# Performance work log

Hardware: AMD Instinct MI355X
Metric: run time of the kernel (lower is better)

The kernel has to match this reference:

```python
import jax, jax.numpy as jnp
import numpy as np
from jax import lax

ANGRES = 5


def _conv(x, w, stride=(1, 1), pad=((1, 1), (1, 1)), dil=(1, 1)):
    return lax.conv_general_dilated(x, w, stride, pad, rhs_dilation=dil,
                                    dimension_numbers=('NCHW', 'OIHW', 'NCHW'))


def _lrelu(x):
    return jnp.where(x >= 0, x, 0.1 * x)


def _block_s(x, w):
    # SAI input: split into 5x5 grid of (sh,sw) views, conv each view, emit MacPI-interleaved layout
    B, C, H, W = x.shape
    sh, sw = H // 5, W // 5
    p = x.reshape(B, C, 5, sh, 5, sw).transpose(0, 2, 4, 1, 3, 5).reshape(B * 25, C, sh, sw)
    y = _conv(p, w).reshape(B, 5, 5, C, sh, sw)
    # (B,bi,bj,C,sh,sw) -> (B,C,sh,bi,sw,bj) -> (B,C,H,W)   [torch permute(0,3,4,1,5,2)]
    return y.transpose(0, 3, 4, 1, 5, 2).reshape(B, C, H, W)


def _block_a(x, w):
    # MacPI input: conv each 5x5 macropixel independently (zero pad at block edges)
    B, C, H, W = x.shape
    nh, nw = H // 5, W // 5
    p = x.reshape(B, C, nh, 5, nw, 5).transpose(0, 2, 4, 1, 3, 5).reshape(B * nh * nw, C, 5, 5)
    y = _conv(p, w)
    return y.reshape(B, nh, nw, C, 5, 5).transpose(0, 3, 1, 4, 2, 5).reshape(B, C, H, W)


def _epi(x, w1, w2, a):
    # EPI conv: [1,3a] kernel, stride [1,a], pad [0,a]; then 1x1 to a*C; then 1D pixel shuffle on W
    y = _lrelu(_conv(x, w1, stride=(1, a), pad=((0, 0), (a, a))))
    y = _lrelu(_conv(y, w2, pad=((0, 0), (0, 0))))
    B, aC, H, Wa = y.shape
    C = aC // a
    return y.reshape(B, a, C, H, Wa).transpose(0, 2, 3, 4, 1).reshape(B, C, H, Wa * a)


def _att_fuse(buf, alpha, gamma, beta, eps=1e-5):
    # covariance-based GLU attention over the N=4 branches
    B, NC, H, W = buf.shape
    N = 4
    C = NC // N
    x5 = buf.reshape(B, N, C, H, W)
    xr = x5.reshape(B, N, C * H * W)
    M = xr.shape[-1]
    xc = xr - jnp.mean(xr, axis=-1, keepdims=True)
    cov = jnp.einsum('bnm,bkm->bnk', xc, xc) * (alpha / (M - 1))  # [B,N,N]
    norm = cov / jnp.sqrt(jnp.mean(cov * cov, axis=(1, 2), keepdims=True) + eps)
    g = gamma * norm + beta
    att = g * jax.nn.sigmoid(g)  # GLU of duplicated halves
    out = jnp.einsum('bnk,bkm->bnm', att, xr).reshape(B, N, C, H, W) + x5
    return out.reshape(B, NC, H, W)


def _mac2sai(x, a):
    B, C, HU, WV = x.shape
    h, w = HU // a, WV // a
    return x.reshape(B, C, a, h, a, w).transpose(0, 1, 3, 5, 2, 4).reshape(B, C, h * a, w * a)


def _tsfefb(x, x1, ws, wa, we1, we2, al, ga, be, wf1, wf2, a):
    feaSpa = _lrelu(_block_s(x1, ws))
    feaAng = _lrelu(_block_a(x, wa))
    feaH = _epi(x, we1, we2, a)
    feaV = jnp.transpose(_epi(jnp.transpose(x, (0, 1, 3, 2)), we1, we2, a), (0, 1, 3, 2))
    buf = jnp.concatenate([feaSpa, feaAng, feaH, feaV], axis=1)
    out = _att_fuse(buf, al, ga, be)
    y = _lrelu(_conv(out, wf1, pad=((0, 0), (0, 0))))
    y = _conv(y, wf2, pad=((a, a), (a, a)), dil=(a, a))
    return y + x


def setup_inputs() -> dict:
    key = jax.random.key(0)
    ks = jax.random.split(key, 12)
    B, C, a, n = 4, 64, ANGRES, 4
    H = W = a * 32  # 160

    def w(k, shape):
        fan_in = float(np.prod(shape[2:]))
        return jax.random.normal(k, shape, jnp.float32) / np.float32(np.sqrt(fan_in))

    return {
        'x': jax.random.normal(ks[0], (B, C, H, W), jnp.float32),
        'x1': jax.random.normal(ks[1], (B, C, H, W), jnp.float32),
        'w_spa': w(ks[2], (n, C, C, 3, 3)),
        'w_ang': w(ks[3], (n, C, C, 3, 3)),
        'w_epi1': w(ks[4], (n, C, C, 1, 3 * a)),
        'w_epi2': w(ks[5], (n, a * C, C, 1, 1)),
        'alpha': jnp.ones((n,), jnp.float32),
        'gamma': 0.1 * jax.random.normal(ks[6], (n,), jnp.float32),
        'beta': 0.1 * jax.random.normal(ks[7], (n,), jnp.float32),
        'w_fuse1': w(ks[8], (n, C, 4 * C, 1, 1)),
        'w_fuse2': w(ks[9], (n, C, C, 3, 3)),
    }


def reference(x, x1, w_spa, w_ang, w_epi1, w_epi2, alpha, gamma, beta, w_fuse1, w_fuse2):
    a = ANGRES
    buf, buf1 = x, x1
    for i in range(w_spa.shape[0]):
        buf = _tsfefb(buf, buf1, w_spa[i], w_ang[i], w_epi1[i], w_epi2[i],
                      alpha[i], gamma[i], beta[i], w_fuse1[i], w_fuse2[i], a)
        buf1 = _mac2sai(buf, a)
    return buf
```

## Files before the change

### kernel.cpp

```cpp
#include <hip/hip_runtime.h>

__device__ __forceinline__ float lrelu(float v){ return v >= 0.f ? v : 0.1f*v; }


__global__ __launch_bounds__(256) void k_spa(const float* __restrict__ buf1, const float* __restrict__ w,
                                             float* __restrict__ out){
  const int P = blockIdx.x;
  const int within = P >> 3, cog = within & 7, tsel = within >> 3;
  const int tg = (P & 7)*25 + tsel;
  const int b = tg / 50, r2 = tg % 50;
  const int view = r2 >> 1, half = r2 & 1;
  const int bi = view / 5, bj = view % 5;
  const int th0 = half*16;
  const int tid = threadIdx.x;
  __shared__ float plane[2][18*38];
  for (int idx=tid; idx<2*18*38; idx+=256) ((float*)plane)[idx]=0.f;
  float acc[2][8];
  #pragma unroll
  for (int k=0;k<2;k++)
    #pragma unroll
    for (int c=0;c<8;c++) acc[k][c]=0.f;
  const float* src = buf1 + (size_t)b*1638400 + bi*32*160 + bj*32;
  const float* wb = w + (size_t)(cog*8)*576;
  const int sr = tid >> 3, sq = (tid & 7)*4;
  const int vr = th0 - 1 + sr;
  const bool rowok = (tid < 144) && ((unsigned)vr < 32u);
  __syncthreads();
  if (rowok)
    *(float4*)&plane[0][sr*38 + 4 + sq] = *(const float4*)(src + vr*160 + sq);
  __syncthreads();
  const int lr = tid >> 5, c = tid & 31;
  for (int ci=0; ci<64; ci++){
    float4 nx;
    const bool ld = rowok && (ci < 63);
    if (ld) nx = *(const float4*)(src + (size_t)(ci+1)*25600 + vr*160 + sq);
    const float* P2 = plane[ci & 1];
    float t0[9], t1[9];
    {
      const float* pp = &P2[lr*38 + c + 3];
      t0[0]=pp[0];  t0[1]=pp[1];  t0[2]=pp[2];
      t0[3]=pp[38]; t0[4]=pp[39]; t0[5]=pp[40];
      t0[6]=pp[76]; t0[7]=pp[77]; t0[8]=pp[78];
      const float* qq = pp + 8*38;
      t1[0]=qq[0];  t1[1]=qq[1];  t1[2]=qq[2];
      t1[3]=qq[38]; t1[4]=qq[39]; t1[5]=qq[40];
      t1[6]=qq[76]; t1[7]=qq[77]; t1[8]=qq[78];
    }
    #pragma unroll
    for (int co=0;co<8;co++){
      const float* wp = wb + (size_t)co*576 + ci*9;
      float w0=wp[0],w1=wp[1],w2=wp[2],w3=wp[3],w4=wp[4],w5=wp[5],w6=wp[6],w7=wp[7],w8=wp[8];
      acc[0][co] += t0[0]*w0+t0[1]*w1+t0[2]*w2+t0[3]*w3+t0[4]*w4
                  + t0[5]*w5+t0[6]*w6+t0[7]*w7+t0[8]*w8;
      acc[1][co] += t1[0]*w0+t1[1]*w1+t1[2]*w2+t1[3]*w3+t1[4]*w4
                  + t1[5]*w5+t1[6]*w6+t1[7]*w7+t1[8]*w8;
    }
    if (ld) *(float4*)&plane[(ci+1)&1][sr*38 + 4 + sq] = nx;
    __syncthreads();
  }
  #pragma unroll
  for (int k=0;k<2;k++){
    int si = th0 + lr + k*8;
    int h = si*5 + bi, wq = c*5 + bj;
    #pragma unroll
    for (int co=0;co<8;co++){
      int ch = b*64 + cog*8 + co;
      out[(size_t)ch*25600 + h*160 + wq] = lrelu(acc[k][co]);
    }
  }
}

__global__ __launch_bounds__(320) void k_ang(const float* __restrict__ bufA, const float* __restrict__ w,
                                             float* __restrict__ out){
  const int P = blockIdx.x;
  const int within = P >> 3, cog = within & 15, tsel = within >> 4;
  const int tg = (P & 7)*8 + tsel;
  const int b = tg >> 4, mip = tg & 15;
  const int tid = threadIdx.x;
  __shared__ float lds[2][2240];
  for (int i=tid; i<2*2240; i+=320) ((float*)lds)[i] = 0.f;

  const int u = tid >> 6, mi_l = (tid >> 5) & 1, mp = tid & 31;
  int offm[3], offa[3];
  #pragma unroll
  for (int du=0; du<3; du++){
    offm[du] = mi_l*896 + (u+du)*128 + mp*4;
    offa[du] = 1792 + mi_l*224 + (u+du)*32 + mp;
  }
  const bool st1 = tid < 80;
  int sdst0[4], sdst1[4];
  const int rr0 = tid/40,       q0 = tid%40;
  const int rr1 = (tid+320)/40, q1 = (tid+320)%40;
  #pragma unroll
  for (int j=0;j<4;j++){
    int g = q0*4+j, mpw = g/5, vw = g - mpw*5;
    int miw = rr0/5, uw = rr0 - miw*5;
    sdst0[j] = (vw<4) ? (miw*896 + (1+uw)*128 + mpw*4 + vw)
                      : (1792 + miw*224 + (1+uw)*32 + mpw);
    g = q1*4+j; mpw = g/5; vw = g - mpw*5;
    miw = rr1/5; uw = rr1 - miw*5;
    sdst1[j] = (vw<4) ? (miw*896 + (1+uw)*128 + mpw*4 + vw)
                      : (1792 + miw*224 + (1+uw)*32 + mpw);
  }
  const float* src = bufA + (size_t)b*1638400 + (size_t)(mip*10)*160;
  const float* wb = w + (size_t)(cog*4)*576;

  float acc[4][5];
  #pragma unroll
  for (int co=0;co<4;co++)
    #pragma unroll
    for (int v=0;v<5;v++) acc[co][v]=0.f;

  __syncthreads();
  {
    float4 x0 = *(const float4*)(src + rr0*160 + q0*4);
    lds[0][sdst0[0]]=x0.x; lds[0][sdst0[1]]=x0.y; lds[0][sdst0[2]]=x0.z; lds[0][sdst0[3]]=x0.w;
    if (st1){
      float4 x1 = *(const float4*)(src + rr1*160 + q1*4);
      lds[0][sdst1[0]]=x1.x; lds[0][sdst1[1]]=x1.y; lds[0][sdst1[2]]=x1.z; lds[0][sdst1[3]]=x1.w;
    }
  }
  __syncthreads();
  for (int ci=0; ci<64; ci++){
    float4 n0, n1;
    if (ci < 63){
      n0 = *(const float4*)(src + (size_t)(ci+1)*25600 + rr0*160 + q0*4);
      if (st1) n1 = *(const float4*)(src + (size_t)(ci+1)*25600 + rr1*160 + q1*4);
    }
    const float* Pb = lds[ci & 1];
    float c[3][5];
    #pragma unroll
    for (int du=0;du<3;du++){
      float4 m = *(const float4*)&Pb[offm[du]];
      c[du][0]=m.x; c[du][1]=m.y; c[du][2]=m.z; c[du][3]=m.w;
      c[du][4]=Pb[offa[du]];
    }
    #pragma unroll
    for (int co=0;co<4;co++){
      const float* wp = wb + (size_t)co*576 + ci*9;
      float w0=wp[0],w1=wp[1],w2=wp[2],w3=wp[3],w4=wp[4],w5=wp[5],w6=wp[6],w7=wp[7],w8=wp[8];
      acc[co][0] += c[0][0]*w1 + c[0][1]*w2
                  + c[1][0]*w4 + c[1][1]*w5
                  + c[2][0]*w7 + c[2][1]*w8;
      acc[co][1] += c[0][0]*w0 + c[0][1]*w1 + c[0][2]*w2
                  + c[1][0]*w3 + c[1][1]*w4 + c[1][2]*w5
                  + c[2][0]*w6 + c[2][1]*w7 + c[2][2]*w8;
      acc[co][2] += c[0][1]*w0 + c[0][2]*w1 + c[0][3]*w2
                  + c[1][1]*w3 + c[1][2]*w4 + c[1][3]*w5
                  + c[2][1]*w6 + c[2][2]*w7 + c[2][3]*w8;
      acc[co][3] += c[0][2]*w0 + c[0][3]*w1 + c[0][4]*w2
                  + c[1][2]*w3 + c[1][3]*w4 + c[1][4]*w5
                  + c[2][2]*w6 + c[2][3]*w7 + c[2][4]*w8;
      acc[co][4] += c[0][3]*w0 + c[0][4]*w1
                  + c[1][3]*w3 + c[1][4]*w4
                  + c[2][3]*w6 + c[2][4]*w7;
    }
    if (ci < 63){
      float* Q = lds[(ci+1)&1];
      Q[sdst0[0]]=n0.x; Q[sdst0[1]]=n0.y; Q[sdst0[2]]=n0.z; Q[sdst0[3]]=n0.w;
      if (st1){ Q[sdst1[0]]=n1.x; Q[sdst1[1]]=n1.y; Q[sdst1[2]]=n1.z; Q[sdst1[3]]=n1.w; }
    }
    __syncthreads();
  }
  const int h = (mip*2 + mi_l)*5 + u;
  const int wc0 = mp*5;
  #pragma unroll
  for (int co=0;co<4;co++){
    int ch = b*64 + cog*4 + co;
    float* op = out + (size_t)ch*25600 + (size_t)h*160 + wc0;
    op[0]=lrelu(acc[co][0]); op[1]=lrelu(acc[co][1]); op[2]=lrelu(acc[co][2]);
    op[3]=lrelu(acc[co][3]); op[4]=lrelu(acc[co][4]);
  }
}

__global__ __launch_bounds__(320) void k_epi(const float* __restrict__ bufA, const float* __restrict__ we1,
                                             const float* __restrict__ we2, float* __restrict__ out){
  const int b = blockIdx.x / 160, hw = blockIdx.x % 160;
  const int tid = threadIdx.x;
  __shared__ float rowp[64*176];
  __shared__ float y1s[64*32];
  for (int ft=tid; ft<2560; ft+=320){
    int ci = ft/40, xq = (ft - ci*40)*4;
    *(float4*)&rowp[ci*176 + 8 + xq] =
      *(const float4*)(bufA + (size_t)b*1638400 + (size_t)ci*25600 + (size_t)hw*160 + xq);
  }
  for (int idx=tid; idx<64*16; idx+=320){
    int ci = idx>>4, j = idx&15;
    rowp[ci*176 + (j<8 ? j : 160+j)] = 0.f;
  }
  __syncthreads();
  if (tid < 256){
    const int co = tid >> 2, wv0 = (tid & 3)*8;
    const int a0 = 2 + wv0*5;
    float acc[8];
    #pragma unroll
    for (int j=0;j<8;j++) acc[j]=0.f;
    const float* wp0 = we1 + (size_t)co*960;
    for (int ci=0; ci<64; ci++){
      float fl[52];
      const float* rp = &rowp[ci*176 + a0];
      #pragma unroll
      for (int m=0;m<26;m++) *(float2*)&fl[2*m] = *(const float2*)&rp[2*m];
      const float* wp = wp0 + ci*15;
      #pragma unroll
      for (int t=0;t<15;t++){
        float wt = wp[t];
        #pragma unroll
        for (int j=0;j<8;j++) acc[j] += fl[1 + j*5 + t]*wt;
      }
    }
    #pragma unroll
    for (int j=0;j<8;j++) y1s[co*32 + wv0 + j] = lrelu(acc[j]);
  }
  __syncthreads();
  {
    const int oc = tid, kk = oc >> 6, c = oc & 63;
    float a2[32];
    #pragma unroll
    for (int wv=0;wv<32;wv++) a2[wv]=0.f;
    const float* wp = we2 + (size_t)oc*64;
    for (int ci=0; ci<64; ci++){
      float wt = wp[ci];
      const float* yp = &y1s[ci*32];
      #pragma unroll
      for (int wv=0; wv<32; wv++) a2[wv] += yp[wv]*wt;
    }
    float* y2s = rowp;
    #pragma unroll
    for (int wv=0; wv<32; wv++) y2s[c*164 + wv*5 + kk] = lrelu(a2[wv]);
  }
  __syncthreads();
  {
    const float* y2s = rowp;
    for (int k=0;k<8;k++){
      int f = (tid + k*320)*4;
      int c = f/160, rr = f - c*160;
      *(float4*)(out + (size_t)(b*64+c)*25600 + (size_t)hw*160 + rr) = *(const float4*)&y2s[c*164+rr];
    }
  }
}

__global__ __launch_bounds__(256) void k_permV(const float* __restrict__ tmp, float* __restrict__ dst){
  const int bc = blockIdx.x;
  const int ti = blockIdx.y / 5, tj = blockIdx.y % 5;
  const int hw0 = ti*32, r0 = tj*32;
  const int lx = threadIdx.x & 31, ly = threadIdx.x >> 5;
  __shared__ float tile[32][33];
  const float* in = tmp + (size_t)bc*25600;
  float* outp = dst + (size_t)bc*25600;
  for (int yy=ly; yy<32; yy+=8)
    tile[yy][lx] = in[(size_t)(hw0+yy)*160 + r0 + lx];
  __syncthreads();
  for (int yy=ly; yy<32; yy+=8)
    outp[(size_t)(r0+yy)*160 + hw0 + lx] = tile[lx][yy];
}

__global__ __launch_bounds__(256) void k_permM(const float* __restrict__ A, float* __restrict__ dst){
  const int bc = blockIdx.x >> 5, hh = blockIdx.x & 31;
  const int tid = threadIdx.x;
  __shared__ float rows[5*160];
  const float* in = A + (size_t)bc*25600;
  if (tid < 200){
    int ai = tid/40, q = (tid - ai*40)*4;
    *(float4*)&rows[ai*160 + q] = *(const float4*)(in + (size_t)(ai*32+hh)*160 + q);
  }
  __syncthreads();
  float* outp = dst + (size_t)bc*25600 + (size_t)hh*800;
  for (int t=tid; t<800; t+=256){
    int ww = t/25, r2 = t - ww*25, ai = r2/5, aj = r2 - ai*5;
    outp[t] = rows[ai*160 + aj*32 + ww];
  }
}

__global__ __launch_bounds__(256) void k_red(const float* __restrict__ b0, const float* __restrict__ b1,
                                             const float* __restrict__ b2, const float* __restrict__ b3,
                                             float* __restrict__ part){
  const int b = blockIdx.y, blk = blockIdx.x;
  const int tid = threadIdx.x;
  const size_t off = (size_t)b*1638400 + (size_t)blk*25600;
  float s0=0,s1=0,s2=0,s3=0;
  float p00=0,p01=0,p02=0,p03=0,p11=0,p12=0,p13=0,p22=0,p23=0,p33=0;
  for (int it=0; it<25; it++){
    size_t m = off + it*1024 + tid*4;
    float4 x0 = *(const float4*)(b0+m);
    float4 x1 = *(const float4*)(b1+m);
    float4 x2 = *(const float4*)(b2+m);
    float4 x3 = *(const float4*)(b3+m);
    s0 += (x0.x+x0.y)+(x0.z+x0.w);
    s1 += (x1.x+x1.y)+(x1.z+x1.w);
    s2 += (x2.x+x2.y)+(x2.z+x2.w);
    s3 += (x3.x+x3.y)+(x3.z+x3.w);
    p00 += x0.x*x0.x+x0.y*x0.y+x0.z*x0.z+x0.w*x0.w;
    p01 += x0.x*x1.x+x0.y*x1.y+x0.z*x1.z+x0.w*x1.w;
    p02 += x0.x*x2.x+x0.y*x2.y+x0.z*x2.z+x0.w*x2.w;
    p03 += x0.x*x3.x+x0.y*x3.y+x0.z*x3.z+x0.w*x3.w;
    p11 += x1.x*x1.x+x1.y*x1.y+x1.z*x1.z+x1.w*x1.w;
    p12 += x1.x*x2.x+x1.y*x2.y+x1.z*x2.z+x1.w*x2.w;
    p13 += x1.x*x3.x+x1.y*x3.y+x1.z*x3.z+x1.w*x3.w;
    p22 += x2.x*x2.x+x2.y*x2.y+x2.z*x2.z+x2.w*x2.w;
    p23 += x2.x*x3.x+x2.y*x3.y+x2.z*x3.z+x2.w*x3.w;
    p33 += x3.x*x3.x+x3.y*x3.y+x3.z*x3.z+x3.w*x3.w;
  }
  float vals[14] = {s0,s1,s2,s3,p00,p01,p02,p03,p11,p12,p13,p22,p23,p33};
  __shared__ float red[4][14];
  int lane = tid & 63, wv = tid >> 6;
  #pragma unroll
  for (int j=0;j<14;j++){
    float v = vals[j];
    #pragma unroll
    for (int o=32;o>0;o>>=1) v += __shfl_down(v,o,64);
    if (lane==0) red[wv][j]=v;
  }
  __syncthreads();
  if (tid<14) part[((size_t)b*64+blk)*16 + tid] = red[0][tid]+red[1][tid]+red[2][tid]+red[3][tid];
}

__global__ __launch_bounds__(256) void k_attW(const float* __restrict__ part,
        const float* __restrict__ alpha, const float* __restrict__ gamma, const float* __restrict__ beta,
        int iblk, const float* __restrict__ wf1, float* __restrict__ Weff){
  const int b = blockIdx.x, tid = threadIdx.x;
  __shared__ float st[14];
  __shared__ float att[16];
  if (tid<14){
    float t=0;
    for (int blk=0;blk<64;blk++) t += part[((size_t)b*64+blk)*16 + tid];
    st[tid]=t;
  }
  __syncthreads();
  if (tid==0){
    const float M = 1638400.f;
    float s[4] = {st[0],st[1],st[2],st[3]};
    float S[4][4];
    S[0][0]=st[4];  S[0][1]=S[1][0]=st[5];  S[0][2]=S[2][0]=st[6];  S[0][3]=S[3][0]=st[7];
    S[1][1]=st[8];  S[1][2]=S[2][1]=st[9];  S[1][3]=S[3][1]=st[10];
    S[2][2]=st[11]; S[2][3]=S[3][2]=st[12]; S[3][3]=st[13];
    float al=alpha[iblk], ga=gamma[iblk], be=beta[iblk];
    float scale = al/(M-1.f);
    float cov[4][4], ss=0.f;
    for (int n=0;n<4;n++) for (int k=0;k<4;k++){
      float c = (S[n][k] - s[n]*s[k]/M)*scale;
      cov[n][k]=c; ss += c*c;
    }
    float rms = sqrtf(ss/16.f + 1e-5f);
    for (int n=0;n<4;n++) for (int k=0;k<4;k++){
      float g = ga*cov[n][k]/rms + be;
      att[n*4+k] = g/(1.f+expf(-g));
    }
  }
  __syncthreads();
  for (int idx=tid; idx<16384; idx+=256){
    int co=idx>>8, kc=idx&255, k=kc>>6, c=kc&63;
    float v = wf1[co*256+kc];
    #pragma unroll
    for (int n=0;n<4;n++) v += att[n*4+k]*wf1[co*256+n*64+c];
    Weff[(size_t)b*16384+idx] = v;
  }
}

__global__ __launch_bounds__(256) void k_fuse1(const float* b0, const float* __restrict__ b1,
                                               const float* __restrict__ b2, const float* __restrict__ b3,
                                               const float* __restrict__ Weff, float* y64){
  const int tile = blockIdx.x, b = blockIdx.y;
  const int px0 = tile*64;
  const int tid = threadIdx.x;
  const int ti = tid >> 4, tj = tid & 15;
  __shared__ float xs[64][68];
  __shared__ float wt[64][68];
  float acc[4][4];
  #pragma unroll
  for (int i=0;i<4;i++)
    #pragma unroll
    for (int j=0;j<4;j++) acc[i][j]=0.f;
  const float* bptr[4] = {b0,b1,b2,b3};
  for (int kb=0; kb<4; kb++){
    const float* xbk = bptr[kb] + (size_t)b*1638400 + px0;
    const float* wb = Weff + (size_t)b*16384 + kb*64;
    __syncthreads();
    for (int idx=tid; idx<4096; idx+=256){
      int kc=idx>>6, px=idx&63;
      xs[kc][px] = xbk[(size_t)kc*25600 + px];
    }
    for (int idx=tid; idx<4096; idx+=256){
      int co=idx>>6, k2=idx&63;
      wt[k2][co] = wb[co*256 + k2];
    }
    __syncthreads();
    for (int k2=0;k2<64;k2++){
      float4 a = *(const float4*)&wt[k2][ti*4];
      float4 v = *(const float4*)&xs[k2][tj*4];
      acc[0][0]+=a.x*v.x; acc[0][1]+=a.x*v.y; acc[0][2]+=a.x*v.z; acc[0][3]+=a.x*v.w;
      acc[1][0]+=a.y*v.x; acc[1][1]+=a.y*v.y; acc[1][2]+=a.y*v.z; acc[1][3]+=a.y*v.w;
      acc[2][0]+=a.z*v.x; acc[2][1]+=a.z*v.y; acc[2][2]+=a.z*v.z; acc[2][3]+=a.z*v.w;
      acc[3][0]+=a.w*v.x; acc[3][1]+=a.w*v.y; acc[3][2]+=a.w*v.z; acc[3][3]+=a.w*v.w;
    }
  }
  #pragma unroll
  for (int i=0;i<4;i++){
    int co = ti*4 + i;
    float4 o = make_float4(lrelu(acc[i][0]), lrelu(acc[i][1]), lrelu(acc[i][2]), lrelu(acc[i][3]));
    *(float4*)(y64 + ((size_t)(b*64+co))*25600 + px0 + tj*4) = o;
  }
}

template<int FINAL>
__global__ __launch_bounds__(256) void k_fuse2(const float* __restrict__ y64, const float* resid,
                                               const float* __restrict__ w, float* outp){
  const int P = blockIdx.x;
  const int within = P >> 3, cog = within & 7, tsel = within >> 3;
  const int tg = (P & 7)*25 + tsel;
  const int b = tg / 50, tile = tg % 50;
  const int th0 = (tile/5)*16, tw0 = (tile%5)*32;
  const int tid = threadIdx.x;
  __shared__ float plane[2][26*44];
  float acc[2][8];
  #pragma unroll
  for (int k=0;k<2;k++)
    #pragma unroll
    for (int c=0;c<8;c++) acc[k][c]=0.f;
  const float* src = y64 + (size_t)b*1638400;
  const float* wb = w + (size_t)(cog*8)*576;
  int soff[5], sdst[5];
  #pragma unroll
  for (int s=0;s<5;s++){
    int idx = tid + s*256;
    int r = idx/42, cc = idx - r*42;
    int gh = th0 + r - 5, gw = tw0 + cc - 5;
    sdst[s] = r*44 + cc;
    soff[s] = ((unsigned)gh < 160u && (unsigned)gw < 160u) ? (gh*160 + gw) : -1;
  }
  const bool s4 = (tid < 68);
  #pragma unroll
  for (int s=0;s<4;s++)
    plane[0][sdst[s]] = (soff[s] >= 0) ? src[soff[s]] : 0.f;
  if (s4) plane[0][sdst[4]] = (soff[4] >= 0) ? src[soff[4]] : 0.f;
  __syncthreads();
  const int lr = tid >> 5, c = tid & 31;
  for (int ci=0; ci<64; ci++){
    float nv[5];
    if (ci < 63){
      const float* s1 = src + (size_t)(ci+1)*25600;
      #pragma unroll
      for (int s=0;s<5;s++) nv[s] = (soff[s] >= 0) ? s1[soff[s]] : 0.f;
    }
    const float* Pb = plane[ci & 1];
    float t0[9], t1[9];
    {
      const float* pp = &Pb[lr*44 + c];
      t0[0]=pp[0];      t0[1]=pp[5];      t0[2]=pp[10];
      t0[3]=pp[220];    t0[4]=pp[225];    t0[5]=pp[230];
      t0[6]=pp[440];    t0[7]=pp[445];    t0[8]=pp[450];
      const float* qq = pp + 8*44;
      t1[0]=qq[0];      t1[1]=qq[5];      t1[2]=qq[10];
      t1[3]=qq[220];    t1[4]=qq[225];    t1[5]=qq[230];
      t1[6]=qq[440];    t1[7]=qq[445];    t1[8]=qq[450];
    }
    #pragma unroll
    for (int co=0;co<8;co++){
      const float* wp = wb + (size_t)co*576 + ci*9;
      float w0=wp[0],w1=wp[1],w2=wp[2],w3=wp[3],w4=wp[4],w5=wp[5],w6=wp[6],w7=wp[7],w8=wp[8];
      acc[0][co] += t0[0]*w0+t0[1]*w1+t0[2]*w2+t0[3]*w3+t0[4]*w4
                  + t0[5]*w5+t0[6]*w6+t0[7]*w7+t0[8]*w8;
      acc[1][co] += t1[0]*w0+t1[1]*w1+t1[2]*w2+t1[3]*w3+t1[4]*w4
                  + t1[5]*w5+t1[6]*w6+t1[7]*w7+t1[8]*w8;
    }
    if (ci < 63){
      float* Q = plane[(ci+1)&1];
      #pragma unroll
      for (int s=0;s<4;s++) Q[sdst[s]] = nv[s];
      if (s4) Q[sdst[4]] = nv[4];
    }
    __syncthreads();
  }
  #pragma unroll
  for (int k=0;k<2;k++){
    int h = th0 + lr + k*8, wq = tw0 + c;
    #pragma unroll
    for (int co=0;co<8;co++){
      int cg = cog*8 + co;
      size_t base = ((size_t)(b*64+cg)*160 + h)*160 + wq;
      outp[base] = acc[k][co] + resid[base];
    }
  }
}

extern "C" void kernel_launch(void* const* d_in, const int* in_sizes, int n_in,
                              void* d_out, int out_size, void* d_ws, size_t ws_size,
                              hipStream_t stream){
  const float* x    = (const float*)d_in[0];
  const float* x1   = (const float*)d_in[1];
  const float* wspa = (const float*)d_in[2];
  const float* wang = (const float*)d_in[3];
  const float* we1  = (const float*)d_in[4];
  const float* we2  = (const float*)d_in[5];
  const float* al   = (const float*)d_in[6];
  const float* ga   = (const float*)d_in[7];
  const float* be   = (const float*)d_in[8];
  const float* wf1  = (const float*)d_in[9];
  const float* wf2  = (const float*)d_in[10];

  char* ws = (char*)d_ws;
  const size_t SLOT = 26214400;
  float* A  = (float*)(ws);
  float* Bv = (float*)(ws +   SLOT);
  float* T1 = (float*)(ws + 2*SLOT);
  float* T2 = (float*)(ws + 3*SLOT);
  float* part = (float*)(ws + 4*SLOT);
  float* Weff = (float*)(ws + 4*SLOT + 16384);
  float* D = (float*)d_out;

  for (int i=0;i<4;i++){
    const float* Asrc  = (i==0) ? x  : (const float*)A;
    const float* B1src = (i==0) ? x1 : (const float*)Bv;
    k_permV<<<dim3(256,25),256,0,stream>>>(Asrc, D);
    k_epi<<<640,320,0,stream>>>(D, we1 + (size_t)i*61440, we2 + (size_t)i*20480, T2);
    k_spa<<<1600,256,0,stream>>>(B1src, wspa + (size_t)i*36864, T1);
    k_permV<<<dim3(256,25),256,0,stream>>>(T2, Bv);
    k_ang<<<1024,320,0,stream>>>(Asrc, wang + (size_t)i*36864, T2);
    k_epi<<<640,320,0,stream>>>(Asrc, we1 + (size_t)i*61440, we2 + (size_t)i*20480, D);
    k_red<<<dim3(64,4),256,0,stream>>>(T1, T2, D, Bv, part);
    k_attW<<<4,256,0,stream>>>(part, al, ga, be, i, wf1 + (size_t)i*16384, Weff);
    k_fuse1<<<dim3(400,4),256,0,stream>>>(T1, T2, D, Bv, Weff, T1);
    if (i<3){
      k_fuse2<0><<<1600,256,0,stream>>>(T1, Asrc, wf2 + (size_t)i*36864, A);
      k_permM<<<8192,256,0,stream>>>(A, Bv);
    } else {
      k_fuse2<1><<<1600,256,0,stream>>>(T1, Asrc, wf2 + (size_t)i*36864, D);
    }
  }
}
```

Measured before the change: 2.912 ms.

## Use padded contiguous LDS rows in k_ang and stage two input channels per sync in k_fuse2

In k_ang the shared-memory staging layout now stores each macropixel row contiguously with 164-float row pitch. Global loads go straight to LDS as float4 stores instead of four scattered scalar stores, and each thread reads its five values per row contiguously. In k_fuse2 the LDS plane buffer grows from two to four planes, so each iteration stages two input channels at once and the number of barriers is halved. This trades extra LDS footprint and registers for fewer syncs and cheaper stores, which may lower occupancy and introduce bank conflicts on the stride-5 reads.

```diff
diff --git a/kernel.cpp b/kernel.cpp
--- a/kernel.cpp
+++ b/kernel.cpp
@@ -77,31 +77,19 @@
   const int tg = (P & 7)*8 + tsel;
   const int b = tg >> 4, mip = tg & 15;
   const int tid = threadIdx.x;
-  __shared__ float lds[2][2240];
-  for (int i=tid; i<2*2240; i+=320) ((float*)lds)[i] = 0.f;
+  __shared__ float lds[2][2296];
+  for (int i=tid; i<2*2296; i+=320) ((float*)lds)[i] = 0.f;
 
   const int u = tid >> 6, mi_l = (tid >> 5) & 1, mp = tid & 31;
-  int offm[3], offa[3];
-  #pragma unroll
-  for (int du=0; du<3; du++){
-    offm[du] = mi_l*896 + (u+du)*128 + mp*4;
-    offa[du] = 1792 + mi_l*224 + (u+du)*32 + mp;
-  }
+  int ro[3];
+  #pragma unroll
+  for (int du=0; du<3; du++)
+    ro[du] = mi_l*1148 + (u+du)*164 + mp*5;
   const bool st1 = tid < 80;
-  int sdst0[4], sdst1[4];
   const int rr0 = tid/40,       q0 = tid%40;
   const int rr1 = (tid+320)/40, q1 = (tid+320)%40;
-  #pragma unroll
-  for (int j=0;j<4;j++){
-    int g = q0*4+j, mpw = g/5, vw = g - mpw*5;
-    int miw = rr0/5, uw = rr0 - miw*5;
-    sdst0[j] = (vw<4) ? (miw*896 + (1+uw)*128 + mpw*4 + vw)
-                      : (1792 + miw*224 + (1+uw)*32 + mpw);
-    g = q1*4+j; mpw = g/5; vw = g - mpw*5;
-    miw = rr1/5; uw = rr1 - miw*5;
-    sdst1[j] = (vw<4) ? (miw*896 + (1+uw)*128 + mpw*4 + vw)
-                      : (1792 + miw*224 + (1+uw)*32 + mpw);
-  }
+  const int dst0 = (rr0/5)*1148 + (1 + rr0%5)*164 + q0*4;
+  const int dst1 = (rr1/5)*1148 + (1 + rr1%5)*164 + q1*4;
   const float* src = bufA + (size_t)b*1638400 + (size_t)(mip*10)*160;
   const float* wb = w + (size_t)(cog*4)*576;
 
@@ -113,12 +101,9 @@
 
   __syncthreads();
   {
-    float4 x0 = *(const float4*)(src + rr0*160 + q0*4);
-    lds[0][sdst0[0]]=x0.x; lds[0][sdst0[1]]=x0.y; lds[0][sdst0[2]]=x0.z; lds[0][sdst0[3]]=x0.w;
-    if (st1){
-      float4 x1 = *(const float4*)(src + rr1*160 + q1*4);
-      lds[0][sdst1[0]]=x1.x; lds[0][sdst1[1]]=x1.y; lds[0][sdst1[2]]=x1.z; lds[0][sdst1[3]]=x1.w;
-    }
+    *(float4*)&lds[0][dst0] = *(const float4*)(src + rr0*160 + q0*4);
+    if (st1)
+      *(float4*)&lds[0][dst1] = *(const float4*)(src + rr1*160 + q1*4);
   }
   __syncthreads();
   for (int ci=0; ci<64; ci++){
@@ -131,9 +116,8 @@
     float c[3][5];
     #pragma unroll
     for (int du=0;du<3;du++){
-      float4 m = *(const float4*)&Pb[offm[du]];
-      c[du][0]=m.x; c[du][1]=m.y; c[du][2]=m.z; c[du][3]=m.w;
-      c[du][4]=Pb[offa[du]];
+      const float* rp = &Pb[ro[du]];
+      c[du][0]=rp[0]; c[du][1]=rp[1]; c[du][2]=rp[2]; c[du][3]=rp[3]; c[du][4]=rp[4];
     }
     #pragma unroll
     for (int co=0;co<4;co++){
@@ -157,8 +141,8 @@
     }
     if (ci < 63){
       float* Q = lds[(ci+1)&1];
-      Q[sdst0[0]]=n0.x; Q[sdst0[1]]=n0.y; Q[sdst0[2]]=n0.z; Q[sdst0[3]]=n0.w;
-      if (st1){ Q[sdst1[0]]=n1.x; Q[sdst1[1]]=n1.y; Q[sdst1[2]]=n1.z; Q[sdst1[3]]=n1.w; }
+      *(float4*)&Q[dst0] = n0;
+      if (st1) *(float4*)&Q[dst1] = n1;
     }
     __syncthreads();
   }
@@ -411,7 +395,7 @@
   const int b = tg / 50, tile = tg % 50;
   const int th0 = (tile/5)*16, tw0 = (tile%5)*32;
   const int tid = threadIdx.x;
-  __shared__ float plane[2][26*44];
+  __shared__ float plane[4][26*44];
   float acc[2][8];
   #pragma unroll
   for (int k=0;k<2;k++)
@@ -430,44 +414,60 @@
   }
   const bool s4 = (tid < 68);
   #pragma unroll
-  for (int s=0;s<4;s++)
+  for (int s=0;s<4;s++){
     plane[0][sdst[s]] = (soff[s] >= 0) ? src[soff[s]] : 0.f;
-  if (s4) plane[0][sdst[4]] = (soff[4] >= 0) ? src[soff[4]] : 0.f;
+    plane[1][sdst[s]] = (soff[s] >= 0) ? src[25600 + soff[s]] : 0.f;
+  }
+  if (s4){
+    plane[0][sdst[4]] = (soff[4] >= 0) ? src[soff[4]] : 0.f;
+    plane[1][sdst[4]] = (soff[4] >= 0) ? src[25600 + soff[4]] : 0.f;
+  }
   __syncthreads();
   const int lr = tid >> 5, c = tid & 31;
-  for (int ci=0; ci<64; ci++){
-    float nv[5];
-    if (ci < 63){
-      const float* s1 = src + (size_t)(ci+1)*25600;
+  const int tap = lr*44 + c;
+  for (int t=0; t<32; t++){
+    const int pp = (t & 1) << 1;
+    float nv[10];
+    if (t < 31){
+      const float* sA = src + (size_t)(2*t+2)*25600;
+      const float* sB = sA + 25600;
       #pragma unroll
-      for (int s=0;s<5;s++) nv[s] = (soff[s] >= 0) ? s1[soff[s]] : 0.f;
-    }
-    const float* Pb = plane[ci & 1];
-    float t0[9], t1[9];
-    {
-      const float* pp = &Pb[lr*44 + c];
-      t0[0]=pp[0];      t0[1]=pp[5];      t0[2]=pp[10];
-      t0[3]=pp[220];    t0[4]=pp[225];    t0[5]=pp[230];
-      t0[6]=pp[440];    t0[7]=pp[445];    t0[8]=pp[450];
-      const float* qq = pp + 8*44;
-      t1[0]=qq[0];      t1[1]=qq[5];      t1[2]=qq[10];
-      t1[3]=qq[220];    t1[4]=qq[225];    t1[5]=qq[230];
-      t1[6]=qq[440];    t1[7]=qq[445];    t1[8]=qq[450];
-    }
-    #pragma unroll
-    for (int co=0;co<8;co++){
-      const float* wp = wb + (size_t)co*576 + ci*9;
-      float w0=wp[0],w1=wp[1],w2=wp[2],w3=wp[3],w4=wp[4],w5=wp[5],w6=wp[6],w7=wp[7],w8=wp[8];
-      acc[0][co] += t0[0]*w0+t0[1]*w1+t0[2]*w2+t0[3]*w3+t0[4]*w4
-                  + t0[5]*w5+t0[6]*w6+t0[7]*w7+t0[8]*w8;
-      acc[1][co] += t1[0]*w0+t1[1]*w1+t1[2]*w2+t1[3]*w3+t1[4]*w4
-                  + t1[5]*w5+t1[6]*w6+t1[7]*w7+t1[8]*w8;
-    }
-    if (ci < 63){
-      float* Q = plane[(ci+1)&1];
+      for (int s=0;s<5;s++){
+        nv[s]   = (soff[s] >= 0) ? sA[soff[s]] : 0.f;
+        nv[5+s] = (soff[s] >= 0) ? sB[soff[s]] : 0.f;
+      }
+    }
+    #pragma unroll
+    for (int h2=0; h2<2; h2++){
+      const int ci = 2*t + h2;
+      const float* Pb = plane[pp + h2];
+      float t0[9], t1[9];
+      {
+        const float* pq = &Pb[tap];
+        t0[0]=pq[0];      t0[1]=pq[5];      t0[2]=pq[10];
+        t0[3]=pq[220];    t0[4]=pq[225];    t0[5]=pq[230];
+        t0[6]=pq[440];    t0[7]=pq[445];    t0[8]=pq[450];
+        const float* qq = pq + 8*44;
+        t1[0]=qq[0];      t1[1]=qq[5];      t1[2]=qq[10];
+        t1[3]=qq[220];    t1[4]=qq[225];    t1[5]=qq[230];
+        t1[6]=qq[440];    t1[7]=qq[445];    t1[8]=qq[450];
+      }
       #pragma unroll
-      for (int s=0;s<4;s++) Q[sdst[s]] = nv[s];
-      if (s4) Q[sdst[4]] = nv[4];
+      for (int co=0;co<8;co++){
+        const float* wp = wb + (size_t)co*576 + ci*9;
+        float w0=wp[0],w1=wp[1],w2=wp[2],w3=wp[3],w4=wp[4],w5=wp[5],w6=wp[6],w7=wp[7],w8=wp[8];
+        acc[0][co] += t0[0]*w0+t0[1]*w1+t0[2]*w2+t0[3]*w3+t0[4]*w4
+                    + t0[5]*w5+t0[6]*w6+t0[7]*w7+t0[8]*w8;
+        acc[1][co] += t1[0]*w0+t1[1]*w1+t1[2]*w2+t1[3]*w3+t1[4]*w4
+                    + t1[5]*w5+t1[6]*w6+t1[7]*w7+t1[8]*w8;
+      }
+    }
+    if (t < 31){
+      float* QA = plane[pp ^ 2];
+      float* QB = plane[(pp ^ 2) + 1];
+      #pragma unroll
+      for (int s=0;s<4;s++){ QA[sdst[s]] = nv[s]; QB[sdst[s]] = nv[5+s]; }
+      if (s4){ QA[sdst[4]] = nv[4]; QB[sdst[4]] = nv[9]; }
     }
     __syncthreads();
   }
```

After: 3.309 ms. 1.14x slower.
